# Performance work log

Hardware: AMD Instinct MI355X
Metric: run time of the kernel (lower is better)

## Reference

```python
import jax, jax.numpy as jnp
import numpy as np
import math

B, T, P, E, H = 4, 64, 256, 512, 8
D = E // H
LN_EPS = 1e-5


def setup_inputs() -> dict:
    key = jax.random.key(0)
    ks = jax.random.split(key, 6)
    s = 0.02  # weight init scale
    return {
        "x": jax.random.normal(ks[0], (B, T, P, E), jnp.float32),
        "Wq": jax.random.normal(ks[1], (E, E), jnp.float32) * s,
        "bq": jnp.zeros((E,), jnp.float32),
        "Wk": jax.random.normal(ks[2], (E, E), jnp.float32) * s,
        "bk": jnp.zeros((E,), jnp.float32),
        "Wv": jax.random.normal(ks[3], (E, E), jnp.float32) * s,
        "bv": jnp.zeros((E,), jnp.float32),
        "Wo": jax.random.normal(ks[4], (E, E), jnp.float32) * s,
        "bo": jnp.zeros((E,), jnp.float32),
        "ln_g": jnp.ones((E,), jnp.float32),
        "ln_b": jnp.zeros((E,), jnp.float32),
    }


def _proj(x, W, b):
    # torch nn.Linear: y = x @ W.T + b
    return jnp.einsum('btpe,fe->btpf', x, W) + b


def _heads(y):
    # b t p (h d) -> b p h t d
    b, t, p, e = y.shape
    return y.reshape(b, t, p, H, D).transpose(0, 2, 3, 1, 4)


def reference(x, Wq, bq, Wk, bk, Wv, bv, Wo, bo, ln_g, ln_b):
    b, t, p, e = x.shape
    q = _heads(_proj(x, Wq, bq))  # [B,P,H,T,D]
    k = _heads(_proj(x, Wk, bk))
    v = _heads(_proj(x, Wv, bv))

    scores = jnp.einsum('bphtd,bphsd->bphts', q, k) / math.sqrt(D)
    causal_mask = jnp.triu(jnp.ones((t, t), dtype=bool), k=1)  # True above diag
    scores = jnp.where(causal_mask, -jnp.inf, scores)
    attn = jax.nn.softmax(scores, axis=-1)
    o = jnp.einsum('bphts,bphsd->bphtd', attn, v)

    # b p h t d -> b t p (h d)
    o = o.transpose(0, 3, 1, 2, 4).reshape(b, t, p, e)
    attn_out = jnp.einsum('btpe,fe->btpf', o, Wo) + bo

    y = x + attn_out
    # AdaptiveNormalizer with conditioning=None -> plain LayerNorm over E
    mu = jnp.mean(y, axis=-1, keepdims=True)
    var = jnp.var(y, axis=-1, keepdims=True)
    return (y - mu) * jax.lax.rsqrt(var + LN_EPS) * ln_g + ln_b
```

## Files before the change

### kernel.cpp

```cpp
#include <hip/hip_runtime.h>
#include <stdint.h>

#define B_ 4
#define T_ 64
#define P_ 256
#define E_ 512
#define H_ 8
#define D_ 64
#define NF 1536
#define MCH 16384

typedef unsigned short u16;
typedef __attribute__((ext_vector_type(8))) __bf16 bf16x8;
typedef __attribute__((ext_vector_type(4))) float f32x4;

__device__ __forceinline__ u16 f2bf(float x) {
  union { float f; uint32_t u; } a; a.f = x;
  uint32_t u = a.u;
  uint32_t r = (u + 0x7FFFu + ((u >> 16) & 1u)) >> 16;
  return (u16)r;
}

__device__ __forceinline__ bf16x8 ld8(const u16* p) {
  union { uint4 u; bf16x8 b; } t;
  t.u = *reinterpret_cast<const uint4*>(p);
  return t.b;
}

typedef __attribute__((address_space(3))) void lds_void;
typedef __attribute__((address_space(1))) void g_void;
__device__ __forceinline__ void gl_lds16(const void* g, void* l) {
  __builtin_amdgcn_global_load_lds((g_void*)g, (lds_void*)l, 16, 0, 0);
}

__device__ __forceinline__ f32x4 mfma16(bf16x8 a, bf16x8 b, f32x4 c) {
  return __builtin_amdgcn_mfma_f32_16x16x32_bf16(a, b, c, 0, 0, 0);
}

#define SBAR() __builtin_amdgcn_s_barrier()

__global__ void cvt_bf16(const float* __restrict__ src, u16* __restrict__ dst, int n8) {
  int i = blockIdx.x * blockDim.x + threadIdx.x;
  if (i >= n8) return;
  const float4* s = reinterpret_cast<const float4*>(src) + (size_t)i * 2;
  float4 a = s[0], b = s[1];
  union { u16 u[8]; uint4 v; } t;
  t.u[0] = f2bf(a.x); t.u[1] = f2bf(a.y); t.u[2] = f2bf(a.z); t.u[3] = f2bf(a.w);
  t.u[4] = f2bf(b.x); t.u[5] = f2bf(b.y); t.u[6] = f2bf(b.z); t.u[7] = f2bf(b.w);
  reinterpret_cast<uint4*>(dst)[i] = t.v;
}

__global__ void cvt_w(const float* __restrict__ Wq, const float* __restrict__ Wk,
                      const float* __restrict__ Wv, const float* __restrict__ Wo,
                      u16* __restrict__ wqkv, u16* __restrict__ wobf) {
  int idx = blockIdx.x * blockDim.x + threadIdx.x;
  int w = idx >> 15;
  int off = idx & 32767;
  const float* s = (w == 0) ? Wq : (w == 1) ? Wk : (w == 2) ? Wv : Wo;
  const float4* sp = reinterpret_cast<const float4*>(s) + (size_t)off * 2;
  float4 a = sp[0], b = sp[1];
  union { u16 u[8]; uint4 v; } t;
  t.u[0] = f2bf(a.x); t.u[1] = f2bf(a.y); t.u[2] = f2bf(a.z); t.u[3] = f2bf(a.w);
  t.u[4] = f2bf(b.x); t.u[5] = f2bf(b.y); t.u[6] = f2bf(b.z); t.u[7] = f2bf(b.w);
  if (w < 3) reinterpret_cast<uint4*>(wqkv)[w * 32768 + off] = t.v;
  else       reinterpret_cast<uint4*>(wobf)[off] = t.v;
}

#define GP_MFMA(MB)                                                         \
  __builtin_amdgcn_s_setprio(1);                                            \
  _Pragma("unroll") for (int i = 0; i < 4; i++)                             \
  _Pragma("unroll") for (int j = 0; j < 4; j++)                             \
    acc[(MB) + i][j] = mfma16(af[i], bfv[j], acc[(MB) + i][j]);             \
  __builtin_amdgcn_s_setprio(0);

#define GP_READA(E, HH, MB)                                                 \
  _Pragma("unroll") for (int i = 0; i < 4; i++)                             \
    af[i] = ld8(ldsA + ((E) * 2 + (HH)) * 8192 +                            \
                (wr * 128 + ((MB) + i) * 16 + l15) * 32 + xr8);

#define GP_READB(E, HH)                                                     \
  _Pragma("unroll") for (int j = 0; j < 4; j++)                             \
    bfv[j] = ld8(ldsB + ((E) * 2 + (HH)) * 8192 +                           \
                 (wc * 64 + j * 16 + l15) * 32 + xr8);

#define GP_KLOOP()                                                          \
  stageA(0, 0, 0); stageB(0, 0, 0);                                         \
  stageA(0, 1, 0); stageB(0, 1, 0);                                         \
  stageA(1, 0, 1); stageB(1, 0, 1);                                         \
  asm volatile("s_waitcnt vmcnt(8)" ::: "memory");                          \
  SBAR();                                                                   \
  _Pragma("unroll 2") for (int s = 0; s < 8; ++s) {                         \
    const int e = s & 1;                                                    \
    bf16x8 af[4], bfv[4];                                                   \
    GP_READA(e, 0, 0)                                                       \
    GP_READB(e, 0)                                                          \
    if (s < 7) stageA(e ^ 1, 1, s + 1);                                     \
    SBAR();                                                                 \
    GP_MFMA(0)                                                              \
    SBAR();                                                                 \
    GP_READA(e, 0, 4)                                                       \
    if (s < 7) stageB(e ^ 1, 1, s + 1);                                     \
    if (s < 7) { asm volatile("s_waitcnt vmcnt(8)" ::: "memory"); }         \
    else       { asm volatile("s_waitcnt vmcnt(0)" ::: "memory"); }         \
    SBAR();                                                                 \
    GP_MFMA(4)                                                              \
    SBAR();                                                                 \
    GP_READA(e, 1, 0)                                                       \
    GP_READB(e, 1)                                                          \
    if (s < 6) stageA(e, 0, s + 2);                                         \
    SBAR();                                                                 \
    GP_MFMA(0)                                                              \
    SBAR();                                                                 \
    GP_READA(e, 1, 4)                                                       \
    if (s < 6) stageB(e, 0, s + 2);                                         \
    if (s < 6)      { asm volatile("s_waitcnt vmcnt(8)" ::: "memory"); }    \
    else if (s == 6){ asm volatile("s_waitcnt vmcnt(4)" ::: "memory"); }    \
    SBAR();                                                                 \
    GP_MFMA(4)                                                              \
    SBAR();                                                                 \
  }

__global__ __launch_bounds__(512, 2) void k1_qkv(
    const u16* __restrict__ xbf,
    const u16* __restrict__ wqkv,
    const float* __restrict__ bq, const float* __restrict__ bk, const float* __restrict__ bv,
    u16* __restrict__ qkv)
{
  __shared__ u16 lds[65536];
  u16* ldsA = lds;
  u16* ldsB = lds + 32768;

  const int tid = threadIdx.x;
  const int lane = tid & 63, wid = tid >> 6;
  const int wr = wid >> 2, wc = wid & 3;
  const int g4 = lane >> 4, l15 = lane & 15;
  const int xr8 = (g4 ^ ((l15 >> 1) & 3)) * 8;

  const int cpx = gridDim.x >> 3;
  const int logical = (blockIdx.x & 7) * cpx + (blockIdx.x >> 3);
  const int m0 = (logical / 6) * 256;
  const int n0 = (logical % 6) * 256;

  const u16* ga = xbf + (size_t)m0 * E_;
  const u16* gb = wqkv + (size_t)n0 * E_;

  const int r0 = tid >> 2;
  const int c0 = ((tid & 3) ^ ((tid >> 3) & 3)) * 8;

  auto stageA = [&](int e, int h, int kt) {
    const int kc = kt * 64 + h * 32;
    u16* base = ldsA + (e * 2 + h) * 8192;
    gl_lds16(ga + (size_t)r0 * E_ + kc + c0, base + wid * 512);
    gl_lds16(ga + (size_t)(r0 + 128) * E_ + kc + c0, base + 4096 + wid * 512);
  };
  auto stageB = [&](int e, int h, int kt) {
    const int kc = kt * 64 + h * 32;
    u16* base = ldsB + (e * 2 + h) * 8192;
    gl_lds16(gb + (size_t)r0 * E_ + kc + c0, base + wid * 512);
    gl_lds16(gb + (size_t)(r0 + 128) * E_ + kc + c0, base + 4096 + wid * 512);
  };

  f32x4 acc[8][4];
#pragma unroll
  for (int i = 0; i < 8; i++)
#pragma unroll
    for (int j = 0; j < 4; j++) { f32x4 z = {0.f, 0.f, 0.f, 0.f}; acc[i][j] = z; }

  GP_KLOOP()

  float bias4[4];
#pragma unroll
  for (int ni = 0; ni < 4; ni++) {
    const int fcol = n0 + wc * 64 + ni * 16 + l15;
    bias4[ni] = fcol < 512 ? bq[fcol] : (fcol < 1024 ? bk[fcol - 512] : bv[fcol - 1024]);
  }
  const int fbase = n0 + wc * 64 + l15;
#pragma unroll
  for (int mi = 0; mi < 8; mi++)
#pragma unroll
    for (int r = 0; r < 4; r++) {
      const size_t row = m0 + wr * 128 + mi * 16 + g4 * 4 + r;
      u16* dst = qkv + row * NF + fbase;
#pragma unroll
      for (int ni = 0; ni < 4; ni++)
        dst[ni * 16] = f2bf(acc[mi][ni][r] + bias4[ni]);
    }
}

__global__ __launch_bounds__(256) void k2_attn(
    const u16* __restrict__ qkv,
    u16* __restrict__ o)
{
  __shared__ u16 Pl[4][64 * 72];
  const int tid = threadIdx.x, lane = tid & 63, wid = tid >> 6;
  const int gw = blockIdx.x * 4 + wid;
  const int b = gw >> 11;
  const int g = gw & 2047;
  const int h = g & 7, p = g >> 3;
  const int g4 = lane >> 4;
  const size_t ts = (size_t)P_ * NF;
  const u16* qb = qkv + (size_t)b * MCH * NF + (size_t)p * NF + h * D_;
  const u16* kb = qb + 512;
  const u16* vb = qb + 1024;
  u16* ob = o + (size_t)b * MCH * E_;

  bf16x8 qf[4][2], kf[4][2];
#pragma unroll
  for (int i = 0; i < 4; i++)
#pragma unroll
    for (int ks = 0; ks < 2; ks++) {
      const int rr = i * 16 + (lane & 15);
      const int dc = ks * 32 + g4 * 8;
      qf[i][ks] = ld8(qb + (size_t)rr * ts + dc);
      kf[i][ks] = ld8(kb + (size_t)rr * ts + dc);
    }
  f32x4 S[4][4];
#pragma unroll
  for (int i = 0; i < 4; i++)
#pragma unroll
    for (int j = 0; j < 4; j++) { f32x4 z = {0.f, 0.f, 0.f, 0.f}; S[i][j] = z; }
#pragma unroll
  for (int ks = 0; ks < 2; ks++)
#pragma unroll
    for (int mi = 0; mi < 4; mi++)
#pragma unroll
      for (int ni = 0; ni < 4; ni++)
        S[mi][ni] = mfma16(qf[mi][ks], kf[ni][ks], S[mi][ni]);

  u16* pw = &Pl[wid][0];
#pragma unroll
  for (int mi = 0; mi < 4; mi++)
#pragma unroll
    for (int r = 0; r < 4; r++) {
      const int t = mi * 16 + g4 * 4 + r;
      float v[4]; float mx = -1e30f;
#pragma unroll
      for (int ni = 0; ni < 4; ni++) {
        const int s = ni * 16 + (lane & 15);
        v[ni] = (s <= t) ? S[mi][ni][r] * 0.125f : -1e30f;
        mx = fmaxf(mx, v[ni]);
      }
      mx = fmaxf(mx, __shfl_xor(mx, 1));
      mx = fmaxf(mx, __shfl_xor(mx, 2));
      mx = fmaxf(mx, __shfl_xor(mx, 4));
      mx = fmaxf(mx, __shfl_xor(mx, 8));
      float sum = 0.f; float pv[4];
#pragma unroll
      for (int ni = 0; ni < 4; ni++) {
        const int s = ni * 16 + (lane & 15);
        pv[ni] = (s <= t) ? __expf(v[ni] - mx) : 0.f;
        sum += pv[ni];
      }
      sum += __shfl_xor(sum, 1);
      sum += __shfl_xor(sum, 2);
      sum += __shfl_xor(sum, 4);
      sum += __shfl_xor(sum, 8);
      const float inv = 1.0f / sum;
#pragma unroll
      for (int ni = 0; ni < 4; ni++) {
        const int s = ni * 16 + (lane & 15);
        pw[t * 72 + s] = f2bf(pv[ni] * inv);
      }
    }
  __syncthreads();

  f32x4 O[4][4];
#pragma unroll
  for (int i = 0; i < 4; i++)
#pragma unroll
    for (int j = 0; j < 4; j++) { f32x4 z = {0.f, 0.f, 0.f, 0.f}; O[i][j] = z; }
#pragma unroll
  for (int ks = 0; ks < 2; ks++) {
    bf16x8 pa[4], vf[4];
#pragma unroll
    for (int mi = 0; mi < 4; mi++)
      pa[mi] = ld8(pw + (mi * 16 + (lane & 15)) * 72 + ks * 32 + g4 * 8);
#pragma unroll
    for (int ni = 0; ni < 4; ni++) {
      union { u16 u[8]; bf16x8 b; } tv;
#pragma unroll
      for (int j = 0; j < 8; j++) {
        const int s = ks * 32 + g4 * 8 + j;
        tv.u[j] = vb[(size_t)s * ts + ni * 16 + (lane & 15)];
      }
      vf[ni] = tv.b;
    }
#pragma unroll
    for (int mi = 0; mi < 4; mi++)
#pragma unroll
      for (int ni = 0; ni < 4; ni++)
        O[mi][ni] = mfma16(pa[mi], vf[ni], O[mi][ni]);
  }
#pragma unroll
  for (int mi = 0; mi < 4; mi++)
#pragma unroll
    for (int ni = 0; ni < 4; ni++)
#pragma unroll
      for (int r = 0; r < 4; r++) {
        const int t = mi * 16 + g4 * 4 + r;
        const int d = ni * 16 + (lane & 15);
        ob[((size_t)t * P_ + p) * E_ + h * D_ + d] = f2bf(O[mi][ni][r]);
      }
}

__global__ __launch_bounds__(512, 2) void k3_gemm(
    const u16* __restrict__ obf,
    const u16* __restrict__ wo,
    const float* __restrict__ bo,
    const float* __restrict__ x,
    u16* __restrict__ yb)
{
  __shared__ u16 lds[65536];
  u16* ldsA = lds;
  u16* ldsB = lds + 32768;

  const int tid = threadIdx.x;
  const int lane = tid & 63, wid = tid >> 6;
  const int wr = wid >> 2, wc = wid & 3;
  const int g4 = lane >> 4, l15 = lane & 15;
  const int xr8 = (g4 ^ ((l15 >> 1) & 3)) * 8;

  const int cpx = gridDim.x >> 3;
  const int logical = (blockIdx.x & 7) * cpx + (blockIdx.x >> 3);
  const int m0 = (logical >> 1) * 256;
  const int n0 = (logical & 1) * 256;

  const u16* ga = obf + (size_t)m0 * E_;
  const u16* gb = wo + (size_t)n0 * E_;

  const int r0 = tid >> 2;
  const int c0 = ((tid & 3) ^ ((tid >> 3) & 3)) * 8;

  auto stageA = [&](int e, int h, int kt) {
    const int kc = kt * 64 + h * 32;
    u16* base = ldsA + (e * 2 + h) * 8192;
    gl_lds16(ga + (size_t)r0 * E_ + kc + c0, base + wid * 512);
    gl_lds16(ga + (size_t)(r0 + 128) * E_ + kc + c0, base + 4096 + wid * 512);
  };
  auto stageB = [&](int e, int h, int kt) {
    const int kc = kt * 64 + h * 32;
    u16* base = ldsB + (e * 2 + h) * 8192;
    gl_lds16(gb + (size_t)r0 * E_ + kc + c0, base + wid * 512);
    gl_lds16(gb + (size_t)(r0 + 128) * E_ + kc + c0, base + 4096 + wid * 512);
  };

  f32x4 acc[8][4];
#pragma unroll
  for (int i = 0; i < 8; i++)
#pragma unroll
    for (int j = 0; j < 4; j++) { f32x4 z = {0.f, 0.f, 0.f, 0.f}; acc[i][j] = z; }

  GP_KLOOP()

  float bias4[4];
#pragma unroll
  for (int ni = 0; ni < 4; ni++)
    bias4[ni] = bo[n0 + wc * 64 + ni * 16 + l15];
  const int fbase = n0 + wc * 64 + l15;
#pragma unroll
  for (int mi = 0; mi < 8; mi++)
#pragma unroll
    for (int r = 0; r < 4; r++) {
      const size_t row = m0 + wr * 128 + mi * 16 + g4 * 4 + r;
      u16* dst = yb + row * E_ + fbase;
      const float* xr = x + row * E_ + fbase;
#pragma unroll
      for (int ni = 0; ni < 4; ni++)
        dst[ni * 16] = f2bf(acc[mi][ni][r] + bias4[ni] + xr[ni * 16]);
    }
}

__global__ __launch_bounds__(256) void k3_ln(
    const u16* __restrict__ yb, const float* __restrict__ lng,
    const float* __restrict__ lnb, float* __restrict__ out)
{
  const int lane = threadIdx.x & 63;
  const size_t row = (size_t)blockIdx.x * 4 + (threadIdx.x >> 6);
  const int c = lane * 8;
  const uint4 d = *reinterpret_cast<const uint4*>(yb + row * E_ + c);
  const uint32_t* dw = reinterpret_cast<const uint32_t*>(&d);
  float f[8];
#pragma unroll
  for (int j = 0; j < 4; j++) {
    union { uint32_t u; float v; } lo, hi;
    lo.u = dw[j] << 16; hi.u = dw[j] & 0xffff0000u;
    f[2 * j] = lo.v; f[2 * j + 1] = hi.v;
  }
  float s = 0.f, q = 0.f;
#pragma unroll
  for (int j = 0; j < 8; j++) { s += f[j]; q += f[j] * f[j]; }
#pragma unroll
  for (int d2 = 1; d2 < 64; d2 <<= 1) { s += __shfl_xor(s, d2); q += __shfl_xor(q, d2); }
  const float mean = s * (1.0f / 512.0f);
  const float var = q * (1.0f / 512.0f) - mean * mean;
  const float rs = rsqrtf(var + 1e-5f);
  float o8[8];
#pragma unroll
  for (int j = 0; j < 8; j++)
    o8[j] = (f[j] - mean) * rs * lng[c + j] + lnb[c + j];
  float4* op = reinterpret_cast<float4*>(out + row * E_ + c);
  op[0] = make_float4(o8[0], o8[1], o8[2], o8[3]);
  op[1] = make_float4(o8[4], o8[5], o8[6], o8[7]);
}

extern "C" void kernel_launch(void* const* d_in, const int* in_sizes, int n_in,
                              void* d_out, int out_size, void* d_ws, size_t ws_size,
                              hipStream_t stream) {
  const float* x   = (const float*)d_in[0];
  const float* Wq  = (const float*)d_in[1];
  const float* bq  = (const float*)d_in[2];
  const float* Wk  = (const float*)d_in[3];
  const float* bk  = (const float*)d_in[4];
  const float* Wv  = (const float*)d_in[5];
  const float* bv  = (const float*)d_in[6];
  const float* Wo  = (const float*)d_in[7];
  const float* bo  = (const float*)d_in[8];
  const float* lng = (const float*)d_in[9];
  const float* lnb = (const float*)d_in[10];
  float* out = (float*)d_out;
  uint8_t* ws = (uint8_t*)d_ws;

  const size_t NEED_BIG = 270532608ULL;
  if (ws_size >= NEED_BIG) {
    u16* wqkv = (u16*)(ws);
    u16* wobf = (u16*)(ws + 1572864);
    u16* xbf  = (u16*)(ws + 2097152);
    u16* qkvc = (u16*)(ws + 69206016);
    u16* obf  = xbf;
    u16* yb   = qkvc;

    cvt_w<<<512, 256, 0, stream>>>(Wq, Wk, Wv, Wo, wqkv, wobf);
    cvt_bf16<<<16384, 256, 0, stream>>>(x, xbf, B_ * MCH * E_ / 8);
    k1_qkv<<<1536, 512, 0, stream>>>(xbf, wqkv, bq, bk, bv, qkvc);
    k2_attn<<<2048, 256, 0, stream>>>(qkvc, obf);
    k3_gemm<<<512, 512, 0, stream>>>(obf, wobf, bo, x, yb);
    k3_ln<<<16384, 256, 0, stream>>>(yb, lng, lnb, out);
  } else {
    u16* xbf  = (u16*)(ws);
    u16* qkvc = (u16*)(ws + 16777216);
    u16* obf  = (u16*)(ws + 67108864);
    u16* wqkv = (u16*)(ws + 83886080);
    u16* wobf = (u16*)(ws + 85458944);
    u16* yb   = qkvc;

    cvt_w<<<512, 256, 0, stream>>>(Wq, Wk, Wv, Wo, wqkv, wobf);
    for (int b = 0; b < B_; ++b) {
      const float* xb = x + (size_t)b * MCH * E_;
      cvt_bf16<<<4096, 256, 0, stream>>>(xb, xbf, MCH * E_ / 8);
      k1_qkv<<<384, 512, 0, stream>>>(xbf, wqkv, bq, bk, bv, qkvc);
      k2_attn<<<512, 256, 0, stream>>>(qkvc, obf);
      k3_gemm<<<128, 512, 0, stream>>>(obf, wobf, bo, xb, yb);
      k3_ln<<<4096, 256, 0, stream>>>(yb, lng, lnb, out + (size_t)b * MCH * E_);
    }
  }
}
```

Measured before the change: 361.1 us.

## Make each QKV GEMM block sweep all six N tiles with a continuous pipeline

The QKV projection kernel now assigns one 256-row M tile per block and loops over all six 256-wide N tiles inside the block. The global-to-LDS prefetch pipeline runs continuously across N tiles, and the epilogue is emitted once per tile. The aim is to drop the per-block pipeline prologue and epilogue and to reuse the A rows across N tiles. In exchange the grid shrinks from 1536 to 256 blocks, which may underfill the 256 CUs at two blocks per CU and serializes each block's stores with its compute.

```diff
diff --git a/kernel.cpp b/kernel.cpp
--- a/kernel.cpp
+++ b/kernel.cpp
@@ -138,53 +138,92 @@
 
   const int cpx = gridDim.x >> 3;
   const int logical = (blockIdx.x & 7) * cpx + (blockIdx.x >> 3);
-  const int m0 = (logical / 6) * 256;
-  const int n0 = (logical % 6) * 256;
+  const int m0 = logical * 256;
 
   const u16* ga = xbf + (size_t)m0 * E_;
-  const u16* gb = wqkv + (size_t)n0 * E_;
-
   const int r0 = tid >> 2;
   const int c0 = ((tid & 3) ^ ((tid >> 3) & 3)) * 8;
 
-  auto stageA = [&](int e, int h, int kt) {
-    const int kc = kt * 64 + h * 32;
+  auto stageA = [&](int e, int h, int gk) {
+    const int kc = (gk & 7) * 64 + h * 32;
     u16* base = ldsA + (e * 2 + h) * 8192;
     gl_lds16(ga + (size_t)r0 * E_ + kc + c0, base + wid * 512);
     gl_lds16(ga + (size_t)(r0 + 128) * E_ + kc + c0, base + 4096 + wid * 512);
   };
-  auto stageB = [&](int e, int h, int kt) {
-    const int kc = kt * 64 + h * 32;
+  auto stageB = [&](int e, int h, int gk) {
+    const int kc = (gk & 7) * 64 + h * 32;
+    const u16* gbp = wqkv + (size_t)((gk >> 3) << 8) * E_;
     u16* base = ldsB + (e * 2 + h) * 8192;
-    gl_lds16(gb + (size_t)r0 * E_ + kc + c0, base + wid * 512);
-    gl_lds16(gb + (size_t)(r0 + 128) * E_ + kc + c0, base + 4096 + wid * 512);
+    gl_lds16(gbp + (size_t)r0 * E_ + kc + c0, base + wid * 512);
+    gl_lds16(gbp + (size_t)(r0 + 128) * E_ + kc + c0, base + 4096 + wid * 512);
   };
 
   f32x4 acc[8][4];
-#pragma unroll
-  for (int i = 0; i < 8; i++)
-#pragma unroll
-    for (int j = 0; j < 4; j++) { f32x4 z = {0.f, 0.f, 0.f, 0.f}; acc[i][j] = z; }
-
-  GP_KLOOP()
-
-  float bias4[4];
-#pragma unroll
-  for (int ni = 0; ni < 4; ni++) {
-    const int fcol = n0 + wc * 64 + ni * 16 + l15;
-    bias4[ni] = fcol < 512 ? bq[fcol] : (fcol < 1024 ? bk[fcol - 512] : bv[fcol - 1024]);
+
+  stageA(0, 0, 0); stageB(0, 0, 0);
+  stageA(0, 1, 0); stageB(0, 1, 0);
+  stageA(1, 0, 1); stageB(1, 0, 1);
+  asm volatile("s_waitcnt vmcnt(8)" ::: "memory");
+  SBAR();
+
+  for (int it = 0; it < 6; ++it) {
+#pragma unroll
+    for (int i = 0; i < 8; i++)
+#pragma unroll
+      for (int j = 0; j < 4; j++) { f32x4 z = {0.f, 0.f, 0.f, 0.f}; acc[i][j] = z; }
+
+#pragma unroll 2
+    for (int s8 = 0; s8 < 8; ++s8) {
+      const int gk = it * 8 + s8;
+      const int e = s8 & 1;
+      bf16x8 af[4], bfv[4];
+      GP_READA(e, 0, 0)
+      GP_READB(e, 0)
+      if (gk < 47) stageA(e ^ 1, 1, gk + 1);
+      SBAR();
+      GP_MFMA(0)
+      SBAR();
+      GP_READA(e, 0, 4)
+      if (gk < 47) { stageB(e ^ 1, 1, gk + 1);
+                     asm volatile("s_waitcnt vmcnt(8)" ::: "memory"); }
+      else         { asm volatile("s_waitcnt vmcnt(0)" ::: "memory"); }
+      SBAR();
+      GP_MFMA(4)
+      SBAR();
+      GP_READA(e, 1, 0)
+      GP_READB(e, 1)
+      if (gk < 46) stageA(e, 0, gk + 2);
+      SBAR();
+      GP_MFMA(0)
+      SBAR();
+      GP_READA(e, 1, 4)
+      if (gk < 46)       { stageB(e, 0, gk + 2);
+                           asm volatile("s_waitcnt vmcnt(8)" ::: "memory"); }
+      else if (gk == 46) { asm volatile("s_waitcnt vmcnt(4)" ::: "memory"); }
+      SBAR();
+      GP_MFMA(4)
+      SBAR();
+    }
+
+    const int n0 = it * 256;
+    float bias4[4];
+#pragma unroll
+    for (int ni = 0; ni < 4; ni++) {
+      const int fcol = n0 + wc * 64 + ni * 16 + l15;
+      bias4[ni] = fcol < 512 ? bq[fcol] : (fcol < 1024 ? bk[fcol - 512] : bv[fcol - 1024]);
+    }
+    const int fbase = n0 + wc * 64 + l15;
+#pragma unroll
+    for (int mi = 0; mi < 8; mi++)
+#pragma unroll
+      for (int r = 0; r < 4; r++) {
+        const size_t row = m0 + wr * 128 + mi * 16 + g4 * 4 + r;
+        u16* dst = qkv + row * NF + fbase;
+#pragma unroll
+        for (int ni = 0; ni < 4; ni++)
+          dst[ni * 16] = f2bf(acc[mi][ni][r] + bias4[ni]);
+      }
   }
-  const int fbase = n0 + wc * 64 + l15;
-#pragma unroll
-  for (int mi = 0; mi < 8; mi++)
-#pragma unroll
-    for (int r = 0; r < 4; r++) {
-      const size_t row = m0 + wr * 128 + mi * 16 + g4 * 4 + r;
-      u16* dst = qkv + row * NF + fbase;
-#pragma unroll
-      for (int ni = 0; ni < 4; ni++)
-        dst[ni * 16] = f2bf(acc[mi][ni][r] + bias4[ni]);
-    }
 }
 
 __global__ __launch_bounds__(256) void k2_attn(
@@ -431,7 +470,7 @@
 
     cvt_w<<<512, 256, 0, stream>>>(Wq, Wk, Wv, Wo, wqkv, wobf);
     cvt_bf16<<<16384, 256, 0, stream>>>(x, xbf, B_ * MCH * E_ / 8);
-    k1_qkv<<<1536, 512, 0, stream>>>(xbf, wqkv, bq, bk, bv, qkvc);
+    k1_qkv<<<256, 512, 0, stream>>>(xbf, wqkv, bq, bk, bv, qkvc);
     k2_attn<<<2048, 256, 0, stream>>>(qkvc, obf);
     k3_gemm<<<512, 512, 0, stream>>>(obf, wobf, bo, x, yb);
     k3_ln<<<16384, 256, 0, stream>>>(yb, lng, lnb, out);
@@ -447,7 +486,7 @@
     for (int b = 0; b < B_; ++b) {
       const float* xb = x + (size_t)b * MCH * E_;
       cvt_bf16<<<4096, 256, 0, stream>>>(xb, xbf, MCH * E_ / 8);
-      k1_qkv<<<384, 512, 0, stream>>>(xbf, wqkv, bq, bk, bv, qkvc);
+      k1_qkv<<<64, 512, 0, stream>>>(xbf, wqkv, bq, bk, bv, qkvc);
       k2_attn<<<512, 256, 0, stream>>>(qkvc, obf);
       k3_gemm<<<128, 512, 0, stream>>>(obf, wobf, bo, xb, yb);
       k3_ln<<<4096, 256, 0, stream>>>(yb, lng, lnb, out + (size_t)b * MCH * E_);
```

After: 432.7 us. +19.8%, slower.

## Shrink QKV GEMM tile to 128x128 with simple double-buffered K loop

Applied to the files above, without the earlier changes.

Replaces the 256x256, 512-thread QKV projection GEMM, which used a hand-scheduled macro pipeline, with a 128x128 tile on 256 threads. The new K loop uses plain double-buffered LDS staging with an XOR swizzle and one barrier per K step. Grid size grows fourfold, giving more blocks and smaller LDS and register footprints for occupancy. In exchange, each block reuses operands less and the carefully interleaved load/MFMA schedule is lost.

```diff
diff --git a/kernel.cpp b/kernel.cpp
--- a/kernel.cpp
+++ b/kernel.cpp
@@ -120,53 +120,74 @@
     SBAR();                                                                 \
   }
 
-__global__ __launch_bounds__(512, 2) void k1_qkv(
+__global__ __launch_bounds__(256, 2) void k1_qkv(
     const u16* __restrict__ xbf,
     const u16* __restrict__ wqkv,
     const float* __restrict__ bq, const float* __restrict__ bk, const float* __restrict__ bv,
     u16* __restrict__ qkv)
 {
-  __shared__ u16 lds[65536];
+  __shared__ u16 lds[32768];
   u16* ldsA = lds;
-  u16* ldsB = lds + 32768;
+  u16* ldsB = lds + 16384;
 
   const int tid = threadIdx.x;
   const int lane = tid & 63, wid = tid >> 6;
-  const int wr = wid >> 2, wc = wid & 3;
+  const int wr = wid >> 1, wc = wid & 1;
   const int g4 = lane >> 4, l15 = lane & 15;
-  const int xr8 = (g4 ^ ((l15 >> 1) & 3)) * 8;
+  const int xrm = l15 & 7;
 
   const int cpx = gridDim.x >> 3;
   const int logical = (blockIdx.x & 7) * cpx + (blockIdx.x >> 3);
-  const int m0 = (logical / 6) * 256;
-  const int n0 = (logical % 6) * 256;
+  const int m0 = (logical / 12) * 128;
+  const int n0 = (logical % 12) * 128;
 
   const u16* ga = xbf + (size_t)m0 * E_;
   const u16* gb = wqkv + (size_t)n0 * E_;
 
-  const int r0 = tid >> 2;
-  const int c0 = ((tid & 3) ^ ((tid >> 3) & 3)) * 8;
-
-  auto stageA = [&](int e, int h, int kt) {
-    const int kc = kt * 64 + h * 32;
-    u16* base = ldsA + (e * 2 + h) * 8192;
-    gl_lds16(ga + (size_t)r0 * E_ + kc + c0, base + wid * 512);
-    gl_lds16(ga + (size_t)(r0 + 128) * E_ + kc + c0, base + 4096 + wid * 512);
+  const int lrow = lane >> 3;
+  const int lcol = ((lane & 7) ^ lrow) * 8;
+
+  auto stage = [&](int e, int kt) {
+    const int k0 = kt * 64;
+#pragma unroll
+    for (int p = 0; p < 4; ++p) {
+      const int ch = wid * 4 + p;
+      const int r = ch * 8 + lrow;
+      gl_lds16(ga + (size_t)r * E_ + k0 + lcol, ldsA + e * 8192 + ch * 512);
+      gl_lds16(gb + (size_t)r * E_ + k0 + lcol, ldsB + e * 8192 + ch * 512);
+    }
   };
-  auto stageB = [&](int e, int h, int kt) {
-    const int kc = kt * 64 + h * 32;
-    u16* base = ldsB + (e * 2 + h) * 8192;
-    gl_lds16(gb + (size_t)r0 * E_ + kc + c0, base + wid * 512);
-    gl_lds16(gb + (size_t)(r0 + 128) * E_ + kc + c0, base + 4096 + wid * 512);
-  };
-
-  f32x4 acc[8][4];
-#pragma unroll
-  for (int i = 0; i < 8; i++)
+
+  f32x4 acc[4][4];
+#pragma unroll
+  for (int i = 0; i < 4; i++)
 #pragma unroll
     for (int j = 0; j < 4; j++) { f32x4 z = {0.f, 0.f, 0.f, 0.f}; acc[i][j] = z; }
 
-  GP_KLOOP()
+  stage(0, 0);
+  __syncthreads();
+  int cur = 0;
+  for (int kt = 0; kt < 8; ++kt) {
+    if (kt < 7) stage(cur ^ 1, kt + 1);
+#pragma unroll
+    for (int ks = 0; ks < 2; ++ks) {
+      const int xc = ((ks * 4 + g4) ^ xrm) * 8;
+      bf16x8 af[4], bfv[4];
+#pragma unroll
+      for (int mi = 0; mi < 4; mi++)
+        af[mi] = ld8(ldsA + cur * 8192 + (wr * 64 + mi * 16 + l15) * 64 + xc);
+#pragma unroll
+      for (int ni = 0; ni < 4; ni++)
+        bfv[ni] = ld8(ldsB + cur * 8192 + (wc * 64 + ni * 16 + l15) * 64 + xc);
+#pragma unroll
+      for (int mi = 0; mi < 4; mi++)
+#pragma unroll
+        for (int ni = 0; ni < 4; ni++)
+          acc[mi][ni] = mfma16(af[mi], bfv[ni], acc[mi][ni]);
+    }
+    __syncthreads();
+    cur ^= 1;
+  }
 
   float bias4[4];
 #pragma unroll
@@ -176,10 +197,10 @@
   }
   const int fbase = n0 + wc * 64 + l15;
 #pragma unroll
-  for (int mi = 0; mi < 8; mi++)
+  for (int mi = 0; mi < 4; mi++)
 #pragma unroll
     for (int r = 0; r < 4; r++) {
-      const size_t row = m0 + wr * 128 + mi * 16 + g4 * 4 + r;
+      const size_t row = m0 + wr * 64 + mi * 16 + g4 * 4 + r;
       u16* dst = qkv + row * NF + fbase;
 #pragma unroll
       for (int ni = 0; ni < 4; ni++)
@@ -431,7 +452,7 @@
 
     cvt_w<<<512, 256, 0, stream>>>(Wq, Wk, Wv, Wo, wqkv, wobf);
     cvt_bf16<<<16384, 256, 0, stream>>>(x, xbf, B_ * MCH * E_ / 8);
-    k1_qkv<<<1536, 512, 0, stream>>>(xbf, wqkv, bq, bk, bv, qkvc);
+    k1_qkv<<<6144, 256, 0, stream>>>(xbf, wqkv, bq, bk, bv, qkvc);
     k2_attn<<<2048, 256, 0, stream>>>(qkvc, obf);
     k3_gemm<<<512, 512, 0, stream>>>(obf, wobf, bo, x, yb);
     k3_ln<<<16384, 256, 0, stream>>>(yb, lng, lnb, out);
@@ -447,7 +468,7 @@
     for (int b = 0; b < B_; ++b) {
       const float* xb = x + (size_t)b * MCH * E_;
       cvt_bf16<<<4096, 256, 0, stream>>>(xb, xbf, MCH * E_ / 8);
-      k1_qkv<<<384, 512, 0, stream>>>(xbf, wqkv, bq, bk, bv, qkvc);
+      k1_qkv<<<1536, 256, 0, stream>>>(xbf, wqkv, bq, bk, bv, qkvc);
       k2_attn<<<512, 256, 0, stream>>>(qkvc, obf);
       k3_gemm<<<128, 512, 0, stream>>>(obf, wobf, bo, xb, yb);
       k3_ln<<<4096, 256, 0, stream>>>(yb, lng, lnb, out + (size_t)b * MCH * E_);
```

New measurement: 370.8 us. 1.03x slower.
